# Optimization experiments

Hardware: AMD Instinct MI355X
Metric: run time of the kernel (lower is better)

The kernel has to match this reference:

```python
import jax, jax.numpy as jnp
import numpy as np
from jax import lax

B, T, C = 4, 2048, 2048
HK, HV = 16, 16
DK, DV = 128, 128
KW = 4  # conv kernel width
KEY_DIM = HK * DK      # 2048
VAL_DIM = HV * DV      # 2048
QKV_DIM = 2 * KEY_DIM + VAL_DIM  # 6144
EPS_RMS = 1e-6
EPS_NORM = 1e-12


def setup_inputs() -> dict:
    key = jax.random.key(0)
    ks = jax.random.split(key, 7)
    s = 0.02
    x = jax.random.normal(ks[0], (B, T, C), dtype=jnp.float32)
    positions = jnp.broadcast_to(jnp.arange(T, dtype=jnp.int64 if jax.config.jax_enable_x64 else jnp.int32), (B, T))
    W_qkvz = jax.random.normal(ks[1], (C, QKV_DIM + VAL_DIM), dtype=jnp.float32) * s
    W_b = jax.random.normal(ks[2], (C, HV), dtype=jnp.float32) * s
    W_a = jax.random.normal(ks[3], (C, HV), dtype=jnp.float32) * s
    conv_w = jax.random.normal(ks[4], (QKV_DIM, 1, KW), dtype=jnp.float32) * 0.1
    norm_w = jnp.ones((DV,), dtype=jnp.float32)
    W_out = jax.random.normal(ks[5], (VAL_DIM, C), dtype=jnp.float32) * s
    return {"x": x, "positions": positions, "W_qkvz": W_qkvz, "W_b": W_b,
            "W_a": W_a, "conv_w": conv_w, "norm_w": norm_w, "W_out": W_out}


def _l2norm(u):
    n = jnp.sqrt(jnp.sum(u * u, axis=-1, keepdims=True))
    return u / jnp.maximum(n, EPS_NORM)


def _forward(x, W_qkvz, W_b, W_a, conv_w, norm_w, W_out):
    qkvz = x @ W_qkvz                               # [B,T,QKV+VAL]
    qkv, z = qkvz[..., :QKV_DIM], qkvz[..., QKV_DIM:]
    z = z.reshape(B, T, HV, DV)
    beta = jax.nn.sigmoid(x @ W_b)                  # [B,T,HV]
    alpha = jax.nn.sigmoid(x @ W_a)                 # [B,T,HV]

    # depthwise causal conv1d (padding K-1 then truncate to T)
    xc = jnp.transpose(qkv, (0, 2, 1))              # [B,QKV_DIM,T]
    xc = lax.conv_general_dilated(xc, conv_w, window_strides=(1,),
                                  padding=[(KW - 1, 0)],
                                  feature_group_count=QKV_DIM,
                                  dimension_numbers=("NCH", "OIH", "NCH"))
    qkv = jnp.transpose(jax.nn.silu(xc), (0, 2, 1))  # [B,T,QKV_DIM]

    q = _l2norm(qkv[..., :KEY_DIM].reshape(B, T, HK, DK))
    k = _l2norm(qkv[..., KEY_DIM:2 * KEY_DIM].reshape(B, T, HK, DK))
    v = qkv[..., 2 * KEY_DIM:].reshape(B, T, HV, DV)

    def step(state, inp):
        q_t, k_t, v_t, b_t, a_t = inp               # [B,H,DK],[B,H,DK],[B,H,DV],[B,H],[B,H]
        state = a_t[:, :, None, None] * state + \
                b_t[:, :, None, None] * (k_t[..., :, None] * v_t[:, :, None, :])
        out = jnp.einsum('bhk,bhkv->bhv', q_t, state)
        return state, out

    state0 = jnp.zeros((B, HK, DK, DV), dtype=x.dtype)
    seq = (jnp.moveaxis(q, 1, 0), jnp.moveaxis(k, 1, 0), jnp.moveaxis(v, 1, 0),
           jnp.moveaxis(beta, 1, 0), jnp.moveaxis(alpha, 1, 0))
    _, outs = lax.scan(step, state0, seq)           # [T,B,H,DV]
    out = jnp.moveaxis(outs, 0, 1)                  # [B,T,H,DV]

    # RMSNorm over head_v_dim (fp32), gated by sigmoid(z)
    of = out.astype(jnp.float32)
    rms = jnp.mean(of * of, axis=-1, keepdims=True)
    out = ((of * lax.rsqrt(rms + EPS_RMS)) * norm_w).astype(out.dtype)
    out = out * jax.nn.sigmoid(z)
    return out.reshape(B, T, VAL_DIM) @ W_out


def reference(x, positions, W_qkvz, W_b, W_a, conv_w, norm_w, W_out):
    return _forward(x, W_qkvz, W_b, W_a, conv_w, norm_w, W_out)
```

## Files before the change

### kernel.cpp

```cpp
#include <hip/hip_runtime.h>
#include <hip/hip_bf16.h>

typedef __bf16 bf16_t;
typedef __attribute__((ext_vector_type(8))) __bf16 bf16x8;
typedef __attribute__((ext_vector_type(4))) float floatx4;


__device__ __forceinline__ void gload16(const void* g, void* l) {
  __builtin_amdgcn_global_load_lds(
      (const __attribute__((address_space(1))) void*)g,
      (__attribute__((address_space(3))) void*)l, 16, 0, 0);
}

__global__ __launch_bounds__(256) void k_cast_bf16(const float* __restrict__ in,
                                                   bf16_t* __restrict__ out) {
  long i = ((long)blockIdx.x * 256 + threadIdx.x) * 8;
  const float4 a = *(const float4*)(in + i);
  const float4 b = *(const float4*)(in + i + 4);
  bf16x8 o;
  o[0] = (bf16_t)a.x; o[1] = (bf16_t)a.y; o[2] = (bf16_t)a.z; o[3] = (bf16_t)a.w;
  o[4] = (bf16_t)b.x; o[5] = (bf16_t)b.y; o[6] = (bf16_t)b.z; o[7] = (bf16_t)b.w;
  *(bf16x8*)(out + i) = o;
}

__global__ void k_transpose_cast(const float* __restrict__ in, bf16_t* __restrict__ out,
                                 int R, int Ccols) {
  __shared__ float tile[32][33];
  int c0 = blockIdx.x * 32, r0 = blockIdx.y * 32;
  for (int i = threadIdx.y; i < 32; i += 8)
    tile[i][threadIdx.x] = in[(long)(r0 + i) * Ccols + c0 + threadIdx.x];
  __syncthreads();
  for (int i = threadIdx.y; i < 32; i += 8)
    out[(long)(c0 + i) * R + r0 + threadIdx.x] = (bf16_t)tile[threadIdx.x][i];
}

__global__ void k_transpose_f32(const float* __restrict__ in, float* __restrict__ out,
                                int R, int Ccols) {
  int r = blockIdx.x * blockDim.x + threadIdx.x;
  if (r < R)
    for (int c = 0; c < Ccols; ++c) out[(long)c * R + r] = in[(long)r * Ccols + c];
}

__global__ __launch_bounds__(256) void k_beta_alpha(const float* __restrict__ x,
                                                    const float* __restrict__ WbT,
                                                    const float* __restrict__ WaT,
                                                    float* __restrict__ beta,
                                                    float* __restrict__ alpha) {
  int row = blockIdx.x;
  __shared__ float xs[2048];
  for (int i = threadIdx.x; i < 2048; i += 256) xs[i] = x[(long)row * 2048 + i];
  __syncthreads();
  int wave = threadIdx.x >> 6, lane = threadIdx.x & 63;
  for (int o = wave * 8; o < wave * 8 + 8; ++o) {
    const float* W = (o < 16) ? (WbT + (long)o * 2048) : (WaT + (long)(o - 16) * 2048);
    float s = 0.f;
    for (int k2 = lane; k2 < 2048; k2 += 64) s += xs[k2] * W[k2];
    for (int off = 32; off; off >>= 1) s += __shfl_down(s, off);
    if (lane == 0) {
      float sig = 1.f / (1.f + expf(-s));
      int b = row >> 11, t = row & 2047;
      int h = (o < 16) ? o : (o - 16);
      float* dst = (o < 16) ? beta : alpha;
      dst[((long)(b * 16 + h)) * 2048 + t] = sig;
    }
  }
}

template <typename OUT_T>
__global__ __launch_bounds__(256) void k_gemm_bt(const bf16_t* __restrict__ A,
                                                 const bf16_t* __restrict__ Bt,
                                                 OUT_T* __restrict__ C, int M, int N, int K,
                                                 int lda) {
  constexpr int BK = 32;
  __shared__ alignas(16) bf16_t As[128 * BK];
  __shared__ alignas(16) bf16_t Bs[128 * BK];
  const int nwgx = gridDim.x;
  const int nwg = nwgx * gridDim.y;
  const int orig = blockIdx.y * nwgx + blockIdx.x;
  const int work = (orig & 7) * (nwg >> 3) + (orig >> 3);
  const int m0 = (work / nwgx) * 128, n0 = (work % nwgx) * 128;

  const int tid = threadIdx.x;
  const int wave = tid >> 6, lane = tid & 63;
  const int wr = wave >> 1, wc = wave & 1;
  const int lrow = lane & 15, lk = (lane >> 4) << 3;
  floatx4 acc[4][4] = {};

  const int srow0 = wave * 32 + (lane >> 2);
  const int scol = (lane & 3) * 8;
  const bf16_t* aptr = A + (long)(m0 + srow0) * lda + scol;
  const bf16_t* bptr = Bt + (long)(n0 + srow0) * K + scol;
  const long rstepA = 16 * (long)lda;
  const long rstepB = 16 * (long)K;
  bf16_t* as0 = &As[(wave * 32) * BK];
  bf16_t* as1 = &As[(wave * 32 + 16) * BK];
  bf16_t* bs0 = &Bs[(wave * 32) * BK];
  bf16_t* bs1 = &Bs[(wave * 32 + 16) * BK];

  for (int k0 = 0; k0 < K; k0 += BK) {
    __syncthreads();
    gload16(aptr + k0, as0);
    gload16(aptr + rstepA + k0, as1);
    gload16(bptr + k0, bs0);
    gload16(bptr + rstepB + k0, bs1);
    __syncthreads();
    bf16x8 af[4], bfr[4];
#pragma unroll
    for (int i = 0; i < 4; i++) af[i] = *(const bf16x8*)&As[(wr * 64 + i * 16 + lrow) * BK + lk];
#pragma unroll
    for (int i = 0; i < 4; i++) bfr[i] = *(const bf16x8*)&Bs[(wc * 64 + i * 16 + lrow) * BK + lk];
#pragma unroll
    for (int mi = 0; mi < 4; mi++)
#pragma unroll
      for (int ni = 0; ni < 4; ni++)
        acc[mi][ni] = __builtin_amdgcn_mfma_f32_16x16x32_bf16(af[mi], bfr[ni], acc[mi][ni], 0, 0, 0);
  }
  const int crow_base = m0 + wr * 64 + (lane >> 4) * 4;
  const int ccol = n0 + wc * 64 + (lane & 15);
#pragma unroll
  for (int mi = 0; mi < 4; mi++)
#pragma unroll
    for (int ni = 0; ni < 4; ni++)
#pragma unroll
      for (int r = 0; r < 4; r++)
        C[(long)(crow_base + mi * 16 + r) * N + ccol + ni * 16] = (OUT_T)acc[mi][ni][r];
}

__global__ __launch_bounds__(256) void k_conv(const bf16_t* __restrict__ qkvz,
                                              const float* __restrict__ conv_w,
                                              bf16_t* __restrict__ q, bf16_t* __restrict__ k,
                                              bf16_t* __restrict__ v) {
  int row = blockIdx.x;
  int b = row >> 11, t = row & 2047;
  __shared__ float ys[6144];
  __shared__ float gsum[32][9];
  __shared__ float norms[32];
  const int c0 = threadIdx.x * 8;
  for (int c8 = c0; c8 < 6144; c8 += 2048) {
    bf16x8 xr[4];
#pragma unroll
    for (int w2 = 0; w2 < 4; ++w2) {
      int tt = t - 3 + w2;
      bf16x8 zr = {};
      xr[w2] = (tt >= 0) ? *(const bf16x8*)&qkvz[((long)(b * 2048 + tt)) * 8192 + c8] : zr;
    }
#pragma unroll
    for (int j = 0; j < 8; ++j) {
      float4 wv = *(const float4*)&conv_w[(c8 + j) * 4];
      float a = (float)xr[0][j] * wv.x + (float)xr[1][j] * wv.y +
                (float)xr[2][j] * wv.z + (float)xr[3][j] * wv.w;
      ys[c8 + j] = a / (1.f + __expf(-a));
    }
  }
  __syncthreads();
  {
    int g = threadIdx.x >> 3, j = threadIdx.x & 7;
    float s = 0.f;
#pragma unroll
    for (int e = 0; e < 16; ++e) {
      float yv = ys[g * 128 + j * 16 + e];
      s += yv * yv;
    }
    gsum[g][j] = s;
  }
  __syncthreads();
  if (threadIdx.x < 32) {
    float s = 0.f;
#pragma unroll
    for (int j = 0; j < 8; j++) s += gsum[threadIdx.x][j];
    norms[threadIdx.x] = 1.f / fmaxf(sqrtf(s), 1e-12f);
  }
  __syncthreads();
  for (int c8 = c0; c8 < 6144; c8 += 2048) {
    float scale;
    bf16_t* dst;
    if (c8 < 2048) {
      int h = c8 >> 7;
      scale = norms[h];
      dst = q + (((long)(b * 16 + h)) * 2048 + t) * 128 + (c8 & 127);
    } else if (c8 < 4096) {
      int h = (c8 - 2048) >> 7;
      scale = norms[16 + h];
      dst = k + (((long)(b * 16 + h)) * 2048 + t) * 128 + (c8 & 127);
    } else {
      scale = 1.f;
      int h = (c8 - 4096) >> 7;
      dst = v + (((long)(b * 16 + h)) * 2048 + t) * 128 + (c8 & 127);
    }
    bf16x8 o;
#pragma unroll
    for (int j = 0; j < 8; ++j) o[j] = (bf16_t)(ys[c8 + j] * scale);
    *(bf16x8*)dst = o;
  }
}

__global__ __launch_bounds__(256) void k_tr_kv(const bf16_t* __restrict__ kv,
                                               const bf16_t* __restrict__ vv,
                                               bf16_t* __restrict__ qkvz) {
  __shared__ bf16_t t_lds[64 * 136];
  int bh = blockIdx.x >> 5, tc = blockIdx.x & 31;
  int t0 = tc * 64;
  int tid = threadIdx.x;
#pragma unroll
  for (int pass = 0; pass < 2; ++pass) {
    const bf16_t* src = (pass == 0 ? kv : vv) + (long)bh * 2048 * 128 + (long)t0 * 128;
    int r = tid >> 2, sc = (tid & 3) * 32;
    bf16x8 x0 = *(const bf16x8*)(src + (long)r * 128 + sc);
    bf16x8 x1 = *(const bf16x8*)(src + (long)r * 128 + sc + 8);
    bf16x8 x2 = *(const bf16x8*)(src + (long)r * 128 + sc + 16);
    bf16x8 x3 = *(const bf16x8*)(src + (long)r * 128 + sc + 24);
    __syncthreads();
    *(bf16x8*)&t_lds[r * 136 + sc] = x0;
    *(bf16x8*)&t_lds[r * 136 + sc + 8] = x1;
    *(bf16x8*)&t_lds[r * 136 + sc + 16] = x2;
    *(bf16x8*)&t_lds[r * 136 + sc + 24] = x3;
    __syncthreads();
    int d = tid >> 1, h2 = tid & 1;
    bf16_t* dst = qkvz + (long)(bh * 128 + d) * 8192 + (pass ? 4096 : 2048) + t0 + h2 * 32;
#pragma unroll
    for (int g = 0; g < 4; ++g) {
      bf16x8 o;
#pragma unroll
      for (int j = 0; j < 8; ++j) o[j] = t_lds[(h2 * 32 + g * 8 + j) * 136 + d];
      *(bf16x8*)(dst + g * 8) = o;
    }
  }
}

__global__ __launch_bounds__(512, 1) void k_scan_chunked(
    const bf16_t* __restrict__ qv, const bf16_t* __restrict__ kv,
    bf16_t* __restrict__ qkvz, float* __restrict__ so_hi,
    const float* __restrict__ beta, const float* __restrict__ alpha) {
  extern __shared__ char smem[];
  bf16_t* q_lds = (bf16_t*)smem;
  bf16_t* kn_lds = q_lds + 8704;
  bf16_t* kT_lds = kn_lds + 8704;
  bf16_t* vT_lds = kT_lds + 9216;
  bf16_t* P_lds = vT_lds + 2304;
  bf16_t* St_lds = P_lds + 4608;
  float* G_lds = (float*)(St_lds + 4352);
  float* bet_lds = G_lds + 64;
  float* w_lds = bet_lds + 64;
  float* eG_lds = w_lds + 64;

  const int bh = blockIdx.x, dvb = blockIdx.y;
  const int b = bh >> 4, h = bh & 15;
  const int tid = threadIdx.x;
  const int w = tid >> 6, l = tid & 63;
  const int l15 = l & 15, lg = l >> 4;
  const int g = w & 1, r = w >> 1;

  const bf16_t* qb = qv + (long)bh * 2048 * 128;
  const bf16_t* kb = kv + (long)bh * 2048 * 128;
  const bf16_t* kTg = qkvz + (long)bh * 128 * 8192 + 2048;
  const bf16_t* vTg = qkvz + (long)(bh * 128 + dvb * 32) * 8192 + 4096;
  const float* bet = beta + (long)bh * 2048;
  const float* alp = alpha + (long)bh * 2048;

  floatx4 streg[2] = {};
  for (int i = tid; i < 2176; i += 512) ((float*)St_lds)[i] = 0.f;
  __syncthreads();

  const int sr = tid >> 3, ssc = (tid & 7) * 16;
  const int sdk = tid >> 2, ssc2 = (tid & 3) * 16;

  for (int c = 0; c < 32; ++c) {
    const int t0 = c * 64;
    {
      const bf16_t* qs = qb + (long)(t0 + sr) * 128 + ssc;
      const bf16_t* ks = kb + (long)(t0 + sr) * 128 + ssc;
      const bf16_t* kts = kTg + (long)sdk * 8192 + t0 + ssc2;
      bf16x8 a0 = *(const bf16x8*)qs, a1 = *(const bf16x8*)(qs + 8);
      bf16x8 b0 = *(const bf16x8*)ks, b1 = *(const bf16x8*)(ks + 8);
      bf16x8 c0 = *(const bf16x8*)kts, c1 = *(const bf16x8*)(kts + 8);
      *(bf16x8*)&q_lds[sr * 136 + ssc] = a0;
      *(bf16x8*)&q_lds[sr * 136 + ssc + 8] = a1;
      *(bf16x8*)&kn_lds[sr * 136 + ssc] = b0;
      *(bf16x8*)&kn_lds[sr * 136 + ssc + 8] = b1;
      *(bf16x8*)&kT_lds[sdk * 72 + ssc2] = c0;
      *(bf16x8*)&kT_lds[sdk * 72 + ssc2 + 8] = c1;
      if (tid < 256) {
        int svr = tid >> 3, svc = (tid & 7) * 8;
        bf16x8 d0 = *(const bf16x8*)(vTg + (long)svr * 8192 + t0 + svc);
        *(bf16x8*)&vT_lds[svr * 72 + svc] = d0;
      }
      if (w == 0) {
        float bsv = bet[t0 + l];
        float la = __logf(alp[t0 + l]);
#pragma unroll
        for (int off = 1; off < 64; off <<= 1) {
          float xup = __shfl_up(la, off);
          if (l >= off) la += xup;
        }
        float ge = __shfl(la, 63);
        G_lds[l] = la;
        bet_lds[l] = bsv;
        w_lds[l] = bsv * __expf(ge - la);
        eG_lds[l] = __expf(la);
      }
    }
    __syncthreads();

    {
      bf16_t* p = &kT_lds[sdk * 72 + ssc2];
      bf16x8 x0 = *(bf16x8*)p, x1 = *(bf16x8*)(p + 8);
#pragma unroll
      for (int j = 0; j < 8; j++) {
        x0[j] = (bf16_t)((float)x0[j] * w_lds[ssc2 + j]);
        x1[j] = (bf16_t)((float)x1[j] * w_lds[ssc2 + 8 + j]);
      }
      *(bf16x8*)p = x0;
      *(bf16x8*)(p + 8) = x1;
    }

    {
      const int mi = w >> 1;
      bf16x8 aq[4];
#pragma unroll
      for (int ks = 0; ks < 4; ks++)
        aq[ks] = *(bf16x8*)&q_lds[(mi * 16 + l15) * 136 + ks * 32 + lg * 8];
#pragma unroll
      for (int sn2 = 0; sn2 < 2; sn2++) {
        const int sn = (w & 1) * 2 + sn2;
        floatx4 sc_ = {0.f, 0.f, 0.f, 0.f};
#pragma unroll
        for (int ks = 0; ks < 4; ks++) {
          bf16x8 bk = *(bf16x8*)&kn_lds[(sn * 16 + l15) * 136 + ks * 32 + lg * 8];
          sc_ = __builtin_amdgcn_mfma_f32_16x16x32_bf16(aq[ks], bk, sc_, 0, 0, 0);
        }
        const int sl = sn * 16 + l15;
        const float gs = G_lds[sl], bs = bet_lds[sl];
#pragma unroll
        for (int rr = 0; rr < 4; rr++) {
          const int tl = mi * 16 + lg * 4 + rr;
          float val = (sl <= tl) ? sc_[rr] * __expf(G_lds[tl] - gs) * bs : 0.f;
          P_lds[tl * 72 + sl] = (bf16_t)val;
        }
      }
    }
    __syncthreads();

    floatx4 acco = {0.f, 0.f, 0.f, 0.f};
    {
      const int rloc = g * 16 + l15;
      bf16x8 av0 = *(bf16x8*)&vT_lds[rloc * 72 + lg * 8];
      bf16x8 av1 = *(bf16x8*)&vT_lds[rloc * 72 + 32 + lg * 8];
      floatx4 f = {0.f, 0.f, 0.f, 0.f};
#pragma unroll
      for (int ks = 0; ks < 4; ks++) {
        bf16x8 aq = *(bf16x8*)&q_lds[(r * 16 + l15) * 136 + ks * 32 + lg * 8];
        bf16x8 bs_ = *(bf16x8*)&St_lds[rloc * 136 + ks * 32 + lg * 8];
        f = __builtin_amdgcn_mfma_f32_16x16x32_bf16(aq, bs_, f, 0, 0, 0);
      }
#pragma unroll
      for (int rr = 0; rr < 4; rr++) f[rr] *= eG_lds[r * 16 + lg * 4 + rr];
#pragma unroll
      for (int ks2 = 0; ks2 < 2; ks2++) {
        bf16x8 ap = *(bf16x8*)&P_lds[(r * 16 + l15) * 72 + ks2 * 32 + lg * 8];
        f = __builtin_amdgcn_mfma_f32_16x16x32_bf16(ap, (ks2 == 0) ? av0 : av1, f, 0, 0, 0);
      }
      acco = f;
      const float dcv = eG_lds[63];
#pragma unroll
      for (int ni = 0; ni < 2; ni++) {
        const int ni2 = r * 2 + ni;
#pragma unroll
        for (int rr = 0; rr < 4; rr++) streg[ni][rr] *= dcv;
        bf16x8 bk0 = *(bf16x8*)&kT_lds[(ni2 * 16 + l15) * 72 + lg * 8];
        bf16x8 bk1 = *(bf16x8*)&kT_lds[(ni2 * 16 + l15) * 72 + 32 + lg * 8];
        streg[ni] = __builtin_amdgcn_mfma_f32_16x16x32_bf16(av0, bk0, streg[ni], 0, 0, 0);
        streg[ni] = __builtin_amdgcn_mfma_f32_16x16x32_bf16(av1, bk1, streg[ni], 0, 0, 0);
      }
    }
    __syncthreads();

#pragma unroll
    for (int ni = 0; ni < 2; ni++) {
      const int ni2 = r * 2 + ni;
#pragma unroll
      for (int rr = 0; rr < 4; rr++)
        St_lds[(g * 16 + lg * 4 + rr) * 136 + ni2 * 16 + l15] = (bf16_t)streg[ni][rr];
    }
    {
      const int dvg = dvb * 32 + g * 16 + l15;
      const int hcol = h * 128 + dvg;
#pragma unroll
      for (int rr = 0; rr < 4; rr++) {
        const int t = t0 + r * 16 + lg * 4 + rr;
        const long row = (long)b * 2048 + t;
        if (hcol < 1024)
          ((float*)qkvz)[row * 4096 + hcol] = acco[rr];
        else
          so_hi[row * 1024 + hcol - 1024] = acco[rr];
      }
    }
  }
}

__global__ __launch_bounds__(256) void k_rmsgate(const float* __restrict__ so_hi,
                                                 bf16_t* __restrict__ qkvz,
                                                 const float* __restrict__ norm_w) {
  long row = blockIdx.x;
  int tid = threadIdx.x;
  int h = tid >> 4, j = tid & 15;
  const float* srow = (h < 8) ? (const float*)qkvz + row * 4096 + h * 128 + j * 8
                              : so_hi + row * 1024 + (h - 8) * 128 + j * 8;
  float xv[8];
  *(float4*)&xv[0] = *(const float4*)srow;
  *(float4*)&xv[4] = *(const float4*)(srow + 4);
  float ss = 0.f;
#pragma unroll
  for (int e = 0; e < 8; e++) ss += xv[e] * xv[e];
  ss += __shfl_xor(ss, 1); ss += __shfl_xor(ss, 2);
  ss += __shfl_xor(ss, 4); ss += __shfl_xor(ss, 8);
  float rinv = rsqrtf(ss * (1.0f / 128.0f) + 1e-6f);
  const bf16_t* zrow = qkvz + row * 8192 + 6144 + h * 128 + j * 8;
  bf16x8 zv = *(const bf16x8*)zrow;
  bf16x8 o;
#pragma unroll
  for (int e = 0; e < 8; e++) {
    float z = (float)zv[e];
    float gate = 1.f / (1.f + __expf(-z));
    o[e] = (bf16_t)(xv[e] * rinv * norm_w[j * 8 + e] * gate);
  }
  *(bf16x8*)(qkvz + row * 8192 + 2048 + h * 128 + j * 8) = o;
}

extern "C" void kernel_launch(void* const* d_in, const int* in_sizes, int n_in,
                              void* d_out, int out_size, void* d_ws, size_t ws_size,
                              hipStream_t stream) {
  const float* x      = (const float*)d_in[0];
  const float* W_qkvz = (const float*)d_in[2];
  const float* W_b    = (const float*)d_in[3];
  const float* W_a    = (const float*)d_in[4];
  const float* conv_w = (const float*)d_in[5];
  const float* norm_w = (const float*)d_in[6];
  const float* W_out  = (const float*)d_in[7];
  float* out = (float*)d_out;
  char* ws = (char*)d_ws;

  bf16_t* qkvz  = (bf16_t*)(ws + 0);
  bf16_t* xb    = (bf16_t*)(ws + 134217728);
  bf16_t* qv    = (bf16_t*)(ws + 134217728);
  bf16_t* WqT   = (bf16_t*)(ws + 167772160);
  bf16_t* kv    = (bf16_t*)(ws + 167772160);
  bf16_t* vv    = (bf16_t*)(ws + 201326592);
  float*  so_hi = (float*)(ws + 201326592);
  bf16_t* WoT   = (bf16_t*)(ws + 234881024);
  float*  WbT   = (float*)(ws + 243269632);
  float*  WaT   = (float*)(ws + 243400704);
  float*  beta  = (float*)(ws + 243531776);
  float*  alpha = (float*)(ws + 244056064);

  if (ws_size < 244580352) return;

  k_cast_bf16<<<8192, 256, 0, stream>>>(x, xb);
  k_transpose_cast<<<dim3(8192 / 32, 2048 / 32), dim3(32, 8), 0, stream>>>(W_qkvz, WqT, 2048, 8192);
  k_transpose_cast<<<dim3(2048 / 32, 2048 / 32), dim3(32, 8), 0, stream>>>(W_out, WoT, 2048, 2048);
  k_transpose_f32<<<8, 256, 0, stream>>>(W_b, WbT, 2048, 16);
  k_transpose_f32<<<8, 256, 0, stream>>>(W_a, WaT, 2048, 16);
  k_beta_alpha<<<8192, 256, 0, stream>>>(x, WbT, WaT, beta, alpha);
  k_gemm_bt<bf16_t><<<dim3(64, 64), 256, 0, stream>>>(xb, WqT, qkvz, 8192, 8192, 2048, 2048);
  k_conv<<<8192, 256, 0, stream>>>(qkvz, conv_w, qv, kv, vv);
  k_tr_kv<<<2048, 256, 0, stream>>>(kv, vv, qkvz);
  k_scan_chunked<<<dim3(64, 4), 512, 76800, stream>>>(qv, kv, qkvz, so_hi, beta, alpha);
  k_rmsgate<<<8192, 256, 0, stream>>>(so_hi, qkvz, norm_w);
  k_gemm_bt<float><<<dim3(16, 64), 256, 0, stream>>>(qkvz + 2048, WoT, out, 8192, 2048, 2048, 8192);
  (void)in_sizes; (void)n_in; (void)out_size;
}
```

Measured before the change: 983.2 us.

## Replace 128x128 GEMM with double-buffered 256x256 tile kernel using swizzled LDS

Both projection GEMMs move from a 128x128-tile, BK=32, single-buffered kernel to a 512-thread kernel. The new kernel uses 256x256 output tiles, a BK of 64 and two LDS buffers (128 KB of dynamic shared memory), with loads for stage k+2 issued after each compute step. LDS rows are XOR-swizzled to avoid bank conflicts on the fragment reads, and MFMA sections raise wave priority. The goal is more data reuse per byte loaded and overlap of global loads with MFMA work. The cost is higher register and LDS pressure, which limits occupancy to one block per CU, and fewer blocks for the output GEMM.

After: 914.9 us. -6.9%, faster.

```diff
diff --git a/kernel.cpp b/kernel.cpp
--- a/kernel.cpp
+++ b/kernel.cpp
@@ -67,63 +67,80 @@
 }
 
 template <typename OUT_T>
-__global__ __launch_bounds__(256) void k_gemm_bt(const bf16_t* __restrict__ A,
-                                                 const bf16_t* __restrict__ Bt,
-                                                 OUT_T* __restrict__ C, int M, int N, int K,
-                                                 int lda) {
-  constexpr int BK = 32;
-  __shared__ alignas(16) bf16_t As[128 * BK];
-  __shared__ alignas(16) bf16_t Bs[128 * BK];
-  const int nwgx = gridDim.x;
-  const int nwg = nwgx * gridDim.y;
-  const int orig = blockIdx.y * nwgx + blockIdx.x;
-  const int work = (orig & 7) * (nwg >> 3) + (orig >> 3);
-  const int m0 = (work / nwgx) * 128, n0 = (work % nwgx) * 128;
-
+__global__ __launch_bounds__(512, 2) void k_gemm256(const bf16_t* __restrict__ A,
+                                                    const bf16_t* __restrict__ Bt,
+                                                    OUT_T* __restrict__ C,
+                                                    int N, int K, int lda) {
+  extern __shared__ char gsm[];
+  const int m0 = blockIdx.y * 256, n0 = blockIdx.x * 256;
   const int tid = threadIdx.x;
-  const int wave = tid >> 6, lane = tid & 63;
-  const int wr = wave >> 1, wc = wave & 1;
-  const int lrow = lane & 15, lk = (lane >> 4) << 3;
-  floatx4 acc[4][4] = {};
-
-  const int srow0 = wave * 32 + (lane >> 2);
-  const int scol = (lane & 3) * 8;
-  const bf16_t* aptr = A + (long)(m0 + srow0) * lda + scol;
-  const bf16_t* bptr = Bt + (long)(n0 + srow0) * K + scol;
-  const long rstepA = 16 * (long)lda;
-  const long rstepB = 16 * (long)K;
-  bf16_t* as0 = &As[(wave * 32) * BK];
-  bf16_t* as1 = &As[(wave * 32 + 16) * BK];
-  bf16_t* bs0 = &Bs[(wave * 32) * BK];
-  bf16_t* bs1 = &Bs[(wave * 32 + 16) * BK];
-
-  for (int k0 = 0; k0 < K; k0 += BK) {
-    __syncthreads();
-    gload16(aptr + k0, as0);
-    gload16(aptr + rstepA + k0, as1);
-    gload16(bptr + k0, bs0);
-    gload16(bptr + rstepB + k0, bs1);
-    __syncthreads();
-    bf16x8 af[4], bfr[4];
-#pragma unroll
-    for (int i = 0; i < 4; i++) af[i] = *(const bf16x8*)&As[(wr * 64 + i * 16 + lrow) * BK + lk];
-#pragma unroll
-    for (int i = 0; i < 4; i++) bfr[i] = *(const bf16x8*)&Bs[(wc * 64 + i * 16 + lrow) * BK + lk];
-#pragma unroll
-    for (int mi = 0; mi < 4; mi++)
-#pragma unroll
-      for (int ni = 0; ni < 4; ni++)
-        acc[mi][ni] = __builtin_amdgcn_mfma_f32_16x16x32_bf16(af[mi], bfr[ni], acc[mi][ni], 0, 0, 0);
-  }
-  const int crow_base = m0 + wr * 64 + (lane >> 4) * 4;
-  const int ccol = n0 + wc * 64 + (lane & 15);
-#pragma unroll
-  for (int mi = 0; mi < 4; mi++)
-#pragma unroll
-    for (int ni = 0; ni < 4; ni++)
-#pragma unroll
-      for (int r = 0; r < 4; r++)
-        C[(long)(crow_base + mi * 16 + r) * N + ccol + ni * 16] = (OUT_T)acc[mi][ni][r];
+  const int w = tid >> 6, l = tid & 63;
+  const int wm = w >> 2, wn = w & 3;
+  const int l15 = l & 15, lg = l >> 4;
+
+  const bf16_t* asrc[4];
+  const bf16_t* bsrc[4];
+  int dofs[4];
+#pragma unroll
+  for (int t = 0; t < 4; ++t) {
+    int c = t * 512 + tid;
+    int row = c >> 3, cs = (c & 7) ^ (row & 7);
+    asrc[t] = A + (long)(m0 + row) * lda + cs * 8;
+    bsrc[t] = Bt + (long)(n0 + row) * K + cs * 8;
+    dofs[t] = c * 16;
+  }
+
+  auto STAGE = [&](int buf, int k0) {
+    char* ab = gsm + buf * 65536;
+    char* bb = ab + 32768;
+#pragma unroll
+    for (int t = 0; t < 4; ++t) {
+      gload16(asrc[t] + k0, ab + dofs[t]);
+      gload16(bsrc[t] + k0, bb + dofs[t]);
+    }
+  };
+
+  floatx4 acc[8][4] = {};
+  STAGE(0, 0);
+  STAGE(1, 64);
+  const int NK = K >> 6;
+  for (int kt = 0; kt < NK; ++kt) {
+    __syncthreads();
+    const char* As_ = gsm + (kt & 1) * 65536;
+    const char* Bs_ = As_ + 32768;
+#pragma unroll
+    for (int ks = 0; ks < 2; ++ks) {
+      bf16x8 af[8], bfr[4];
+#pragma unroll
+      for (int mi = 0; mi < 8; ++mi) {
+        const int r = wm * 128 + mi * 16 + l15;
+        af[mi] = *(const bf16x8*)(As_ + r * 128 + ((((ks << 2) + lg) ^ (r & 7)) << 4));
+      }
+#pragma unroll
+      for (int ni = 0; ni < 4; ++ni) {
+        const int r = wn * 64 + ni * 16 + l15;
+        bfr[ni] = *(const bf16x8*)(Bs_ + r * 128 + ((((ks << 2) + lg) ^ (r & 7)) << 4));
+      }
+      __builtin_amdgcn_s_setprio(1);
+#pragma unroll
+      for (int mi = 0; mi < 8; ++mi)
+#pragma unroll
+        for (int ni = 0; ni < 4; ++ni)
+          acc[mi][ni] = __builtin_amdgcn_mfma_f32_16x16x32_bf16(af[mi], bfr[ni], acc[mi][ni], 0, 0, 0);
+      __builtin_amdgcn_s_setprio(0);
+    }
+    __syncthreads();
+    if (kt + 2 < NK) STAGE(kt & 1, (kt + 2) << 6);
+  }
+  const int crow0 = m0 + wm * 128 + lg * 4;
+  const int ccol = n0 + wn * 64 + l15;
+#pragma unroll
+  for (int mi = 0; mi < 8; ++mi)
+#pragma unroll
+    for (int ni = 0; ni < 4; ++ni)
+#pragma unroll
+      for (int r = 0; r < 4; ++r)
+        C[(long)(crow0 + mi * 16 + r) * N + ccol + ni * 16] = (OUT_T)acc[mi][ni][r];
 }
 
 __global__ __launch_bounds__(256) void k_conv(const bf16_t* __restrict__ qkvz,
@@ -460,11 +477,11 @@
   k_transpose_f32<<<8, 256, 0, stream>>>(W_b, WbT, 2048, 16);
   k_transpose_f32<<<8, 256, 0, stream>>>(W_a, WaT, 2048, 16);
   k_beta_alpha<<<8192, 256, 0, stream>>>(x, WbT, WaT, beta, alpha);
-  k_gemm_bt<bf16_t><<<dim3(64, 64), 256, 0, stream>>>(xb, WqT, qkvz, 8192, 8192, 2048, 2048);
+  k_gemm256<bf16_t><<<dim3(32, 32), 512, 131072, stream>>>(xb, WqT, qkvz, 8192, 2048, 2048);
   k_conv<<<8192, 256, 0, stream>>>(qkvz, conv_w, qv, kv, vv);
   k_tr_kv<<<2048, 256, 0, stream>>>(kv, vv, qkvz);
   k_scan_chunked<<<dim3(64, 4), 512, 76800, stream>>>(qv, kv, qkvz, so_hi, beta, alpha);
   k_rmsgate<<<8192, 256, 0, stream>>>(so_hi, qkvz, norm_w);
-  k_gemm_bt<float><<<dim3(16, 64), 256, 0, stream>>>(qkvz + 2048, WoT, out, 8192, 2048, 2048, 8192);
+  k_gemm256<float><<<dim3(8, 32), 512, 131072, stream>>>(qkvz + 2048, WoT, out, 2048, 2048, 8192);
   (void)in_sizes; (void)n_in; (void)out_size;
 }
```
